# Optimization experiments

Hardware: AMD Instinct MI355X
Metric: run time of the kernel (lower is better)

## Reference

```python
import jax, jax.numpy as jnp
import numpy as np

N = 50000
E = 800000
IN_C, OUT_C, K = 96, 16, 3
L1 = IN_C - (IN_C - OUT_C) // 3            # 70
L2 = IN_C - (2 * (IN_C - OUT_C)) // 3      # 43


def setup_inputs() -> dict:
    key = jax.random.key(0)
    ks = jax.random.split(key, 12)
    x = jax.random.normal(ks[0], (N, IN_C), dtype=jnp.float32)
    edge_index = jax.random.randint(ks[1], (2, E), 0, N, dtype=jnp.int64)

    def glorot(k, shape):
        fan_in, fan_out = shape[-2], shape[-1]
        lim = jnp.sqrt(6.0 / (fan_in + fan_out)).astype(jnp.float32)
        return jax.random.uniform(k, shape, jnp.float32, -lim, lim)

    W1 = glorot(ks[2], (K + 1, IN_C, L1)); b1 = jnp.zeros((L1,), jnp.float32)
    W2 = glorot(ks[3], (K + 1, L1, L2));   b2 = jnp.zeros((L2,), jnp.float32)
    Wmu = glorot(ks[4], (L2, OUT_C));      bmu = jnp.zeros((OUT_C,), jnp.float32)
    Wls = glorot(ks[5], (L2, OUT_C));      bls = jnp.zeros((OUT_C,), jnp.float32)
    return {"x": x, "edge_index": edge_index, "W1": W1, "b1": b1,
            "W2": W2, "b2": b2, "Wmu": Wmu, "bmu": bmu, "Wls": Wls, "bls": bls}


def _norm_no_self_loops(row, col):
    # gcn_norm, add_self_loops=False (TAGConv default)
    deg = jax.ops.segment_sum(jnp.ones((E,), jnp.float32), col, num_segments=N)
    dis = jnp.where(deg > 0, jax.lax.rsqrt(jnp.maximum(deg, 1.0)), 0.0)
    return dis[row] * dis[col]  # [E]


def _tag_conv(x, W, b, row, col, norm):
    # out = sum_k A_hat^k x W_k + b
    out = x @ W[0]
    h = x
    for k in range(1, K + 1):
        h = jax.ops.segment_sum(norm[:, None] * h[row], col, num_segments=N)
        out = out + h @ W[k]
    return out + b


def _gcn_conv(x, W, b, row, col, dis2):
    # gcn_norm with self-loops: dis2 = (deg+1)^{-1/2}
    y = x @ W
    norm = dis2[row] * dis2[col]
    agg = jax.ops.segment_sum(norm[:, None] * y[row], col, num_segments=N)
    return agg + (dis2 * dis2)[:, None] * y + b  # self-loop term + bias


def reference(x, edge_index, W1, b1, W2, b2, Wmu, bmu, Wls, bls):
    row, col = edge_index[0], edge_index[1]
    norm = _norm_no_self_loops(row, col)
    h = jax.nn.relu(_tag_conv(x, W1, b1, row, col, norm))
    h = jax.nn.relu(_tag_conv(h, W2, b2, row, col, norm))
    deg = jax.ops.segment_sum(jnp.ones((E,), jnp.float32), col, num_segments=N)
    dis2 = jax.lax.rsqrt(deg + 1.0)  # self-loops added -> deg+1 > 0
    mu = _gcn_conv(h, Wmu, bmu, row, col, dis2)
    logstd = _gcn_conv(h, Wls, bls, row, col, dis2)
    return mu, logstd
```

## Files before the change

### kernel.cpp

```cpp
#include <hip/hip_runtime.h>
#include <hip/hip_fp16.h>

static constexpr int NN  = 50000;
static constexpr int EE  = 800000;
static constexpr int CIN = 96;
static constexpr int L1C = 70, S1 = 72;
static constexpr int L2C = 43, S2P = 48;

static constexpr int NT1 = 18, KS1 = 3;
static constexpr int NT2 = 12, KS2 = 3;
static constexpr int NTH = 2,  KSH = 2;
static constexpr int NU1 = NT1 * KS1 * 64 * 4;
static constexpr int NU2 = NT2 * KS2 * 64 * 4;
static constexpr int NUH = NTH * KSH * 64 * 4;
static constexpr int TUW = NU1 + NU2 + NUH;
static constexpr int NBF = 288 + 192;

static constexpr int NSLICE = 8;
static constexpr int SLICEN = NN / NSLICE;

typedef short bf16x8 __attribute__((ext_vector_type(8)));
typedef float f32x4  __attribute__((ext_vector_type(4)));

__device__ __forceinline__ float bf_lo(unsigned int u) {
    return __uint_as_float(u << 16);
}
__device__ __forceinline__ float bf_hi(unsigned int u) {
    return __uint_as_float(u & 0xffff0000u);
}
__device__ __forceinline__ unsigned int bf_rne_bits(float f) {
    unsigned int u = __float_as_uint(f);
    return u + 0x7fffu + ((u >> 16) & 1u);
}
__device__ __forceinline__ unsigned int pack_bf(float a, float b) {
    return (bf_rne_bits(a) >> 16) | (bf_rne_bits(b) & 0xffff0000u);
}
__device__ __forceinline__ void unpack_bf8(uint4 q, float* f) {
    f[0] = bf_lo(q.x); f[1] = bf_hi(q.x); f[2] = bf_lo(q.y); f[3] = bf_hi(q.y);
    f[4] = bf_lo(q.z); f[5] = bf_hi(q.z); f[6] = bf_lo(q.w); f[7] = bf_hi(q.w);
}

__device__ __forceinline__ int rec_src(unsigned int p) { return (int)(p & 0xffffu); }
__device__ __forceinline__ float rec_w(unsigned int p) {
    return __half2float(__ushort_as_half((unsigned short)(p >> 16)));
}


__global__ void init_kernel(const float* __restrict__ W1, const float* __restrict__ b1,
                            const float* __restrict__ W2, const float* __restrict__ b2,
                            const float* __restrict__ Wmu, const float* __restrict__ Wls,
                            unsigned int* __restrict__ wB, float* __restrict__ bB,
                            int* __restrict__ deg) {
    int i = blockIdx.x * blockDim.x + threadIdx.x;
    if (i < NN) deg[i] = 0;
    if (i < TUW) {
        float v0 = 0.f, v1 = 0.f;
        if (i < NU1) {
            int frag = i >> 2, j = i & 3;
            int l = frag & 63, ts = frag >> 6;
            int s = ts % 3, t = ts / 3;
            int col = t * 16 + (l & 15);
            int kb  = s * 32 + (l >> 4) * 8 + j * 2;
            int img = col / S1, cin = col - img * S1;
            if (cin < L1C) {
                const float* Wp = W1 + ((size_t)img * CIN + kb) * L1C + cin;
                v0 = Wp[0];
                v1 = Wp[L1C];
            }
        } else if (i < NU1 + NU2) {
            int u = i - NU1;
            int frag = u >> 2, j = u & 3;
            int l = frag & 63, ts = frag >> 6;
            int s = ts % 3, t = ts / 3;
            int col = t * 16 + (l & 15);
            int kb  = s * 32 + (l >> 4) * 8 + j * 2;
            int img = col / S2P, cin = col - img * S2P;
            if (cin < L2C) {
                const float* Wp = W2 + ((size_t)img * L1C + kb) * L2C + cin;
                if (kb < L1C)     v0 = Wp[0];
                if (kb + 1 < L1C) v1 = Wp[L2C];
            }
        } else {
            int u = i - NU1 - NU2;
            int frag = u >> 2, j = u & 3;
            int l = frag & 63, ts = frag >> 6;
            int s = ts & 1, t = ts >> 1;
            int col = t * 16 + (l & 15);
            int kb  = s * 32 + (l >> 4) * 8 + j * 2;
            const float* Wsel = (col < 16) ? (Wmu + col) : (Wls + (col - 16));
            if (kb < L2C)     v0 = Wsel[kb * 16];
            if (kb + 1 < L2C) v1 = Wsel[(kb + 1) * 16];
        }
        wB[i] = pack_bf(v0, v1);
    } else if (i < TUW + NBF) {
        int j = i - TUW;
        float v = 0.f;
        if (j < 288) { if (j < L1C) v = b1[j]; }
        else { int c = j - 288; if (c < L2C) v = b2[c]; }
        bB[j] = v;
    }
}

__global__ void hist_kernel(const int* __restrict__ row, const int* __restrict__ col,
                            int* __restrict__ deg, unsigned int* __restrict__ rr, int E) {
    int e = blockIdx.x * blockDim.x + threadIdx.x;
    if (e < E) {
        int c = col[e];
        int rk = atomicAdd(&deg[c], 1);
        rr[e] = ((unsigned int)rk << 16) | (unsigned int)row[e];
    }
}

static constexpr int SB = 256;

__global__ void reduce_kernel(const int* __restrict__ deg, int* __restrict__ bsum, int n) {
    __shared__ int sd[SB];
    int i = blockIdx.x * SB + threadIdx.x;
    sd[threadIdx.x] = (i < n) ? deg[i] : 0;
    __syncthreads();
    for (int s = SB / 2; s > 0; s >>= 1) {
        if (threadIdx.x < s) sd[threadIdx.x] += sd[threadIdx.x + s];
        __syncthreads();
    }
    if (threadIdx.x == 0) bsum[blockIdx.x] = sd[0];
}

__global__ void block_scan_kernel(const int* __restrict__ deg, const int* __restrict__ bsum,
                                  int* __restrict__ off,
                                  float* __restrict__ dis, float* __restrict__ dis2,
                                  int n, int nb) {
    __shared__ int sd[SB];
    __shared__ int bofs;
    int t = threadIdx.x;
    sd[t] = (t < nb && t < (int)blockIdx.x) ? bsum[t] : 0;
    __syncthreads();
    for (int s = SB / 2; s > 0; s >>= 1) {
        if (t < s) sd[t] += sd[t + s];
        __syncthreads();
    }
    if (t == 0) bofs = sd[0];
    __syncthreads();
    int i = blockIdx.x * SB + t;
    int v = (i < n) ? deg[i] : 0;
    sd[t] = v;
    __syncthreads();
    for (int s = 1; s < SB; s <<= 1) {
        int tv = (t >= s) ? sd[t - s] : 0;
        __syncthreads();
        sd[t] += tv;
        __syncthreads();
    }
    if (i < n) {
        int e = bofs + sd[t] - v;
        off[i] = e;
        dis[i]  = (v > 0) ? rsqrtf((float)v) : 0.0f;
        dis2[i] = rsqrtf((float)v + 1.0f);
        if (i == n - 1) off[n] = e + v;
    }
}

__global__ void fill_kernel(const int* __restrict__ col, const unsigned int* __restrict__ rr,
                            const float* __restrict__ dis, const int* __restrict__ off,
                            unsigned int* __restrict__ eTag, int E) {
    int s = blockIdx.x & (NSLICE - 1);
    int nlo = s * SLICEN, nhi = nlo + SLICEN;
    int stride = (gridDim.x >> 3) * blockDim.x;
    for (int e = (blockIdx.x >> 3) * blockDim.x + threadIdx.x; e < E; e += stride) {
        int c = col[e];
        if (c >= nlo && c < nhi) {
            unsigned int u = rr[e];
            int r = (int)(u & 0xffffu);
            int pos = off[c] + (int)(u >> 16);
            unsigned short h = __half_as_ushort(__float2half(dis[r] * dis[c]));
            eTag[pos] = (unsigned int)r | ((unsigned int)h << 16);
        }
    }
}

template <int C, bool HASADD, bool RELU>
__global__ void aggw_kernel(const unsigned short* __restrict__ in, const unsigned short* addv,
                            unsigned short* out, const int* __restrict__ off,
                            const unsigned int* __restrict__ ep, int n) {
    constexpr int TPN = C / 8;
    int t = blockIdx.x * blockDim.x + threadIdx.x;
    if (t >= n * TPN) return;
    int node = t / TPN;
    int cc = (t - node * TPN) * 8;
    int beg = off[node], end = off[node + 1];
    float a0[8], a1[8];
    #pragma unroll
    for (int j = 0; j < 8; ++j) { a0[j] = 0.f; a1[j] = 0.f; }
    int e = beg;
    for (; e + 4 <= end; e += 4) {
        unsigned int p0 = ep[e], p1 = ep[e + 1], p2 = ep[e + 2], p3 = ep[e + 3];
        float w0 = rec_w(p0), w1 = rec_w(p1), w2 = rec_w(p2), w3 = rec_w(p3);
        uint4 q0 = *reinterpret_cast<const uint4*>(in + (size_t)rec_src(p0) * C + cc);
        uint4 q1 = *reinterpret_cast<const uint4*>(in + (size_t)rec_src(p1) * C + cc);
        uint4 q2 = *reinterpret_cast<const uint4*>(in + (size_t)rec_src(p2) * C + cc);
        uint4 q3 = *reinterpret_cast<const uint4*>(in + (size_t)rec_src(p3) * C + cc);
        float f[8];
        unpack_bf8(q0, f);
        #pragma unroll
        for (int j = 0; j < 8; ++j) a0[j] += w0 * f[j];
        unpack_bf8(q1, f);
        #pragma unroll
        for (int j = 0; j < 8; ++j) a1[j] += w1 * f[j];
        unpack_bf8(q2, f);
        #pragma unroll
        for (int j = 0; j < 8; ++j) a0[j] += w2 * f[j];
        unpack_bf8(q3, f);
        #pragma unroll
        for (int j = 0; j < 8; ++j) a1[j] += w3 * f[j];
    }
    for (; e < end; ++e) {
        unsigned int p = ep[e];
        float w = rec_w(p);
        uint4 q = *reinterpret_cast<const uint4*>(in + (size_t)rec_src(p) * C + cc);
        float f[8];
        unpack_bf8(q, f);
        #pragma unroll
        for (int j = 0; j < 8; ++j) a0[j] += w * f[j];
    }
    float r[8];
    #pragma unroll
    for (int j = 0; j < 8; ++j) r[j] = a0[j] + a1[j];
    if constexpr (HASADD) {
        uint4 qa = *reinterpret_cast<const uint4*>(addv + (size_t)node * C + cc);
        float f[8];
        unpack_bf8(qa, f);
        #pragma unroll
        for (int j = 0; j < 8; ++j) r[j] += f[j];
    }
    if constexpr (RELU) {
        #pragma unroll
        for (int j = 0; j < 8; ++j) r[j] = fmaxf(r[j], 0.f);
    }
    uint4 o;
    o.x = pack_bf(r[0], r[1]); o.y = pack_bf(r[2], r[3]);
    o.z = pack_bf(r[4], r[5]); o.w = pack_bf(r[6], r[7]);
    *reinterpret_cast<uint4*>(out + (size_t)node * C + cc) = o;
}

__global__ void agg_gcn_final_kernel(const unsigned short* __restrict__ yh,
                                     const int* __restrict__ off,
                                     const unsigned int* __restrict__ ep,
                                     const float* __restrict__ dis2,
                                     const float* __restrict__ bmu,
                                     const float* __restrict__ bls,
                                     float* __restrict__ outp, int n) {
    int t = blockIdx.x * blockDim.x + threadIdx.x;
    if (t >= n * 4) return;
    int node = t >> 2;
    int cc = (t & 3) * 8;
    int beg = off[node], end = off[node + 1];
    float a0[8], a1[8];
    #pragma unroll
    for (int j = 0; j < 8; ++j) { a0[j] = 0.f; a1[j] = 0.f; }
    int e = beg;
    for (; e + 2 <= end; e += 2) {
        int s0 = rec_src(ep[e]), s1 = rec_src(ep[e + 1]);
        float w0 = dis2[s0], w1 = dis2[s1];
        uint4 q0 = *reinterpret_cast<const uint4*>(yh + (size_t)s0 * 32 + cc);
        uint4 q1 = *reinterpret_cast<const uint4*>(yh + (size_t)s1 * 32 + cc);
        float f[8];
        unpack_bf8(q0, f);
        #pragma unroll
        for (int j = 0; j < 8; ++j) a0[j] += w0 * f[j];
        unpack_bf8(q1, f);
        #pragma unroll
        for (int j = 0; j < 8; ++j) a1[j] += w1 * f[j];
    }
    for (; e < end; ++e) {
        int s = rec_src(ep[e]);
        float w = dis2[s];
        uint4 q = *reinterpret_cast<const uint4*>(yh + (size_t)s * 32 + cc);
        float f[8];
        unpack_bf8(q, f);
        #pragma unroll
        for (int j = 0; j < 8; ++j) a0[j] += w * f[j];
    }
    float d = dis2[node];
    uint4 qy = *reinterpret_cast<const uint4*>(yh + (size_t)node * 32 + cc);
    float yv[8];
    unpack_bf8(qy, yv);
    const float* bp = (cc < 16) ? (bmu + cc) : (bls + (cc - 16));
    float r[8];
    #pragma unroll
    for (int j = 0; j < 8; ++j)
        r[j] = d * (a0[j] + a1[j]) + d * d * yv[j] + bp[j];
    size_t o = (cc < 16) ? ((size_t)node * 16 + cc)
                         : ((size_t)n * 16 + (size_t)node * 16 + (cc - 16));
    *reinterpret_cast<float4*>(outp + o) = make_float4(r[0], r[1], r[2], r[3]);
    *reinterpret_cast<float4*>(outp + o + 4) = make_float4(r[4], r[5], r[6], r[7]);
}

template <int KS, int NT, int INS, int OIMG, bool CONV, bool BIAS>
__launch_bounds__(256)
__global__ void gemm_kernel(const void* __restrict__ Xv,
                            const unsigned int* __restrict__ Wp,
                            const float* __restrict__ bv,
                            unsigned short* __restrict__ o0,
                            unsigned short* __restrict__ o1,
                            unsigned short* __restrict__ o2,
                            unsigned short* __restrict__ o3,
                            int n) {
    constexpr int WFR = NT * KS * 64;
    constexpr int XFR = KS * 256;
    __shared__ __align__(16) unsigned int Wl[WFR * 4];
    __shared__ __align__(16) unsigned int Xl[(CONV ? 2 : 1) * XFR * 4];

    const int tid = threadIdx.x;
    const int mb = blockIdx.x * 64;

    {
        const uint4* s4 = reinterpret_cast<const uint4*>(Wp);
        uint4* d4 = reinterpret_cast<uint4*>(Wl);
        for (int i = tid; i < WFR; i += 256) d4[i] = s4[i];
    }
    {
        uint4* dx = reinterpret_cast<uint4*>(Xl);
        const int l = tid & 63, w = (tid >> 6) & 3;
        const int m = mb + w * 16 + (l & 15);
        #pragma unroll
        for (int s = 0; s < KS; ++s) {
            int p = s * 256 + tid;
            int k0 = s * 32 + (l >> 4) * 8;
            if constexpr (CONV) {
                bool ok = (m < n);
                const float4* xp = reinterpret_cast<const float4*>(
                    (const float*)Xv + (size_t)m * INS + k0);
                float4 aa = ok ? xp[0] : make_float4(0.f, 0.f, 0.f, 0.f);
                float4 bb = ok ? xp[1] : make_float4(0.f, 0.f, 0.f, 0.f);
                float xv[8] = {aa.x, aa.y, aa.z, aa.w, bb.x, bb.y, bb.z, bb.w};
                unsigned int hb[4], lb[4];
                #pragma unroll
                for (int j = 0; j < 4; ++j) {
                    float a0 = xv[2 * j], a1 = xv[2 * j + 1];
                    unsigned int h0 = bf_rne_bits(a0) & 0xffff0000u;
                    unsigned int h1 = bf_rne_bits(a1) & 0xffff0000u;
                    float r0 = a0 - __uint_as_float(h0);
                    float r1 = a1 - __uint_as_float(h1);
                    hb[j] = (h0 >> 16) | h1;
                    lb[j] = pack_bf(r0, r1);
                }
                dx[p]       = make_uint4(hb[0], hb[1], hb[2], hb[3]);
                dx[XFR + p] = make_uint4(lb[0], lb[1], lb[2], lb[3]);
            } else {
                uint4 v = make_uint4(0u, 0u, 0u, 0u);
                if (m < n && k0 + 8 <= INS)
                    v = *reinterpret_cast<const uint4*>(
                        (const unsigned short*)Xv + (size_t)m * INS + k0);
                dx[p] = v;
            }
        }
    }
    __syncthreads();

    const int w = tid >> 6, lane = tid & 63;
    const int ln = lane & 15, lg = lane >> 4;
    const bf16x8* Wf = reinterpret_cast<const bf16x8*>(Wl);
    const bf16x8* Xf = reinterpret_cast<const bf16x8*>(Xl);

    f32x4 acc[NT];
    #pragma unroll
    for (int t = 0; t < NT; ++t) {
        float b = 0.f;
        if constexpr (BIAS) b = bv[t * 16 + ln];
        acc[t] = (f32x4){b, b, b, b};
    }
    #pragma unroll
    for (int s = 0; s < KS; ++s) {
        bf16x8 ah = Xf[s * 256 + w * 64 + lane];
        bf16x8 al;
        if constexpr (CONV) al = Xf[XFR + s * 256 + w * 64 + lane];
        #pragma unroll
        for (int t = 0; t < NT; ++t) {
            bf16x8 bw = Wf[(t * KS + s) * 64 + lane];
            acc[t] = __builtin_amdgcn_mfma_f32_16x16x32_bf16(ah, bw, acc[t], 0, 0, 0);
            if constexpr (CONV)
                acc[t] = __builtin_amdgcn_mfma_f32_16x16x32_bf16(al, bw, acc[t], 0, 0, 0);
        }
    }
    const int rbase = mb + w * 16 + lg * 4;
    #pragma unroll
    for (int t = 0; t < NT; ++t) {
        int c = t * 16 + ln;
        int img = c / OIMG;
        int colin = c - img * OIMG;
        unsigned short* ob = (img == 0) ? o0 : (img == 1) ? o1 : (img == 2) ? o2 : o3;
        #pragma unroll
        for (int r = 0; r < 4; ++r) {
            int m = rbase + r;
            if (m < n)
                ob[(size_t)m * OIMG + colin] =
                    (unsigned short)(bf_rne_bits(acc[t][r]) >> 16);
        }
    }
}


extern "C" void kernel_launch(void* const* d_in, const int* in_sizes, int n_in,
                              void* d_out, int out_size, void* d_ws, size_t ws_size,
                              hipStream_t stream) {
    const float* x   = (const float*)d_in[0];
    const int*   ei  = (const int*)d_in[1];
    const float* W1  = (const float*)d_in[2];
    const float* b1  = (const float*)d_in[3];
    const float* W2  = (const float*)d_in[4];
    const float* b2  = (const float*)d_in[5];
    const float* Wmu = (const float*)d_in[6];
    const float* bmu = (const float*)d_in[7];
    const float* Wls = (const float*)d_in[8];
    const float* bls = (const float*)d_in[9];
    float* out = (float*)d_out;

    const int N = NN, E = EE;
    const int* row = ei;
    const int* col = ei + E;

    char* p = (char*)d_ws;
    auto alloc = [&](size_t bytes) -> char* {
        char* r = p;
        p += (bytes + 255) & ~(size_t)255;
        return r;
    };
    int*   deg    = (int*)alloc((size_t)N * 4);
    int*   off    = (int*)alloc((size_t)(N + 1) * 4);
    int*   bsum   = (int*)alloc((size_t)256 * 4);
    float* dis    = (float*)alloc((size_t)N * 4);
    float* dis2   = (float*)alloc((size_t)N * 4);
    unsigned int* wB = (unsigned int*)alloc((size_t)TUW * 4);
    float* bB     = (float*)alloc((size_t)NBF * 4);
    unsigned int* eTag = (unsigned int*)alloc((size_t)E * 4);
    unsigned int* rr   = (unsigned int*)alloc((size_t)E * 4);
    unsigned short* y0 = (unsigned short*)alloc((size_t)N * S1 * 2);
    unsigned short* y1 = (unsigned short*)alloc((size_t)N * S1 * 2);
    unsigned short* y2 = (unsigned short*)alloc((size_t)N * S1 * 2);
    unsigned short* y3 = (unsigned short*)alloc((size_t)N * S1 * 2);
    unsigned short* u0 = (unsigned short*)alloc((size_t)N * S2P * 2);
    unsigned short* u1 = (unsigned short*)alloc((size_t)N * S2P * 2);
    unsigned short* u2 = (unsigned short*)alloc((size_t)N * S2P * 2);
    unsigned short* u3 = (unsigned short*)alloc((size_t)N * S2P * 2);
    unsigned short* yh = (unsigned short*)alloc((size_t)N * 32 * 2);

    const unsigned int* W1b = wB;
    const unsigned int* W2b = wB + NU1;
    const unsigned int* Whb = wB + NU1 + NU2;
    const float* bv1 = bB;
    const float* bv2 = bB + 288;

    const int B = 256;
    int gE = (E + B - 1) / B;
    int nb = (N + SB - 1) / SB;

    init_kernel<<<nb, B, 0, stream>>>(W1, b1, W2, b2, Wmu, Wls, wB, bB, deg);
    hist_kernel<<<gE, B, 0, stream>>>(row, col, deg, rr, E);
    reduce_kernel<<<nb, SB, 0, stream>>>(deg, bsum, N);
    block_scan_kernel<<<nb, SB, 0, stream>>>(deg, bsum, off, dis, dis2, N, nb);
    fill_kernel<<<3200, B, 0, stream>>>(col, rr, dis, off, eTag, E);

    int gmm  = (N + 63) / 64;
    int ga72 = (N * (S1 / 8) + B - 1) / B;
    int ga48 = (N * (S2P / 8) + B - 1) / B;
    int gaF  = (N * 4 + B - 1) / B;

    gemm_kernel<3, 9, CIN, S1, true, true ><<<gmm, B, 0, stream>>>(
        x, W1b, bv1, y0, y1, y2, y3, N);
    gemm_kernel<3, 9, CIN, S1, true, false><<<gmm, B, 0, stream>>>(
        x, W1b + NU1 / 2, nullptr, y2, y3, y2, y3, N);
    aggw_kernel<S1, true, false><<<ga72, B, 0, stream>>>(y3, y2, y2, off, eTag, N);
    aggw_kernel<S1, true, false><<<ga72, B, 0, stream>>>(y2, y1, y1, off, eTag, N);
    aggw_kernel<S1, true, true ><<<ga72, B, 0, stream>>>(y1, y0, y0, off, eTag, N);

    gemm_kernel<3, 12, S1, S2P, false, true><<<gmm, B, 0, stream>>>(
        y0, W2b, bv2, u0, u1, u2, u3, N);
    aggw_kernel<S2P, true, false><<<ga48, B, 0, stream>>>(u3, u2, u2, off, eTag, N);
    aggw_kernel<S2P, true, false><<<ga48, B, 0, stream>>>(u2, u1, u1, off, eTag, N);
    aggw_kernel<S2P, true, true ><<<ga48, B, 0, stream>>>(u1, u0, u0, off, eTag, N);

    gemm_kernel<2, 2, S2P, 32, false, false><<<gmm, B, 0, stream>>>(
        u0, Whb, nullptr, yh, yh, yh, yh, N);
    agg_gcn_final_kernel<<<gaF, B, 0, stream>>>(yh, off, eTag, dis2, bmu, bls, out, N);
}
```

Baseline: 320.6 us.

## Sort nodes by degree into bins and aggregate in permuted order

Builds a 64-bin degree histogram during the scan, computes per-block bin offsets with global atomics, and writes a degree-sorted node permutation in a new kernel. All aggregation kernels then index nodes through this permutation so lanes in a wavefront process nodes with similar edge counts, reducing loop divergence. The cost is an extra kernel, extra atomics, and scattered node-row accesses for offsets, residual adds and outputs instead of contiguous ones.

```diff
diff --git a/kernel.cpp b/kernel.cpp
--- a/kernel.cpp
+++ b/kernel.cpp
@@ -50,9 +50,10 @@
                             const float* __restrict__ W2, const float* __restrict__ b2,
                             const float* __restrict__ Wmu, const float* __restrict__ Wls,
                             unsigned int* __restrict__ wB, float* __restrict__ bB,
-                            int* __restrict__ deg) {
+                            int* __restrict__ deg, int* __restrict__ gBin) {
     int i = blockIdx.x * blockDim.x + threadIdx.x;
     if (i < NN) deg[i] = 0;
+    if (i < 64) gBin[i] = 0;
     if (i < TUW) {
         float v0 = 0.f, v1 = 0.f;
         if (i < NU1) {
@@ -128,11 +129,14 @@
 __global__ void block_scan_kernel(const int* __restrict__ deg, const int* __restrict__ bsum,
                                   int* __restrict__ off,
                                   float* __restrict__ dis, float* __restrict__ dis2,
+                                  int* __restrict__ gBin, int* __restrict__ blockBase,
                                   int n, int nb) {
     __shared__ int sd[SB];
+    __shared__ int hb[64];
     __shared__ int bofs;
     int t = threadIdx.x;
     sd[t] = (t < nb && t < (int)blockIdx.x) ? bsum[t] : 0;
+    if (t < 64) hb[t] = 0;
     __syncthreads();
     for (int s = SB / 2; s > 0; s >>= 1) {
         if (t < s) sd[t] += sd[t + s];
@@ -142,6 +146,7 @@
     __syncthreads();
     int i = blockIdx.x * SB + t;
     int v = (i < n) ? deg[i] : 0;
+    if (i < n) atomicAdd(&hb[min(v, 63)], 1);
     sd[t] = v;
     __syncthreads();
     for (int s = 1; s < SB; s <<= 1) {
@@ -156,6 +161,32 @@
         dis[i]  = (v > 0) ? rsqrtf((float)v) : 0.0f;
         dis2[i] = rsqrtf((float)v + 1.0f);
         if (i == n - 1) off[n] = e + v;
+    }
+    if (t < 64) {
+        int c = hb[t];
+        blockBase[blockIdx.x * 64 + t] = (c > 0) ? atomicAdd(&gBin[t], c) : 0;
+    }
+}
+
+__global__ void perm_kernel(const int* __restrict__ deg, const int* __restrict__ gBin,
+                            const int* __restrict__ blockBase, int* __restrict__ perm,
+                            int n) {
+    __shared__ int binStart[64];
+    __shared__ int cur[64];
+    int t = threadIdx.x;
+    if (t < 64) { binStart[t] = gBin[t]; cur[t] = 0; }
+    __syncthreads();
+    if (t == 0) {
+        int s = 0;
+        #pragma unroll
+        for (int b = 0; b < 64; ++b) { int c = binStart[b]; binStart[b] = s; s += c; }
+    }
+    __syncthreads();
+    int i = blockIdx.x * SB + t;
+    if (i < n) {
+        int b = min(deg[i], 63);
+        int r = atomicAdd(&cur[b], 1);
+        perm[binStart[b] + blockBase[blockIdx.x * 64 + b] + r] = i;
     }
 }
 
@@ -180,12 +211,14 @@
 template <int C, bool HASADD, bool RELU>
 __global__ void aggw_kernel(const unsigned short* __restrict__ in, const unsigned short* addv,
                             unsigned short* out, const int* __restrict__ off,
-                            const unsigned int* __restrict__ ep, int n) {
+                            const unsigned int* __restrict__ ep,
+                            const int* __restrict__ perm, int n) {
     constexpr int TPN = C / 8;
     int t = blockIdx.x * blockDim.x + threadIdx.x;
     if (t >= n * TPN) return;
-    int node = t / TPN;
-    int cc = (t - node * TPN) * 8;
+    int g = t / TPN;
+    int node = perm[g];
+    int cc = (t - g * TPN) * 8;
     int beg = off[node], end = off[node + 1];
     float a0[8], a1[8];
     #pragma unroll
@@ -247,10 +280,11 @@
                                      const float* __restrict__ dis2,
                                      const float* __restrict__ bmu,
                                      const float* __restrict__ bls,
+                                     const int* __restrict__ perm,
                                      float* __restrict__ outp, int n) {
     int t = blockIdx.x * blockDim.x + threadIdx.x;
     if (t >= n * 4) return;
-    int node = t >> 2;
+    int node = perm[t >> 2];
     int cc = (t & 3) * 8;
     int beg = off[node], end = off[node + 1];
     float a0[8], a1[8];
@@ -433,6 +467,9 @@
     float* bB     = (float*)alloc((size_t)NBF * 4);
     unsigned int* eTag = (unsigned int*)alloc((size_t)E * 4);
     unsigned int* rr   = (unsigned int*)alloc((size_t)E * 4);
+    int*   gBin   = (int*)alloc((size_t)64 * 4);
+    int*   blockBase = (int*)alloc((size_t)256 * 64 * 4);
+    int*   perm   = (int*)alloc((size_t)N * 4);
     unsigned short* y0 = (unsigned short*)alloc((size_t)N * S1 * 2);
     unsigned short* y1 = (unsigned short*)alloc((size_t)N * S1 * 2);
     unsigned short* y2 = (unsigned short*)alloc((size_t)N * S1 * 2);
@@ -453,10 +490,12 @@
     int gE = (E + B - 1) / B;
     int nb = (N + SB - 1) / SB;
 
-    init_kernel<<<nb, B, 0, stream>>>(W1, b1, W2, b2, Wmu, Wls, wB, bB, deg);
+    init_kernel<<<nb, B, 0, stream>>>(W1, b1, W2, b2, Wmu, Wls, wB, bB, deg, gBin);
     hist_kernel<<<gE, B, 0, stream>>>(row, col, deg, rr, E);
     reduce_kernel<<<nb, SB, 0, stream>>>(deg, bsum, N);
-    block_scan_kernel<<<nb, SB, 0, stream>>>(deg, bsum, off, dis, dis2, N, nb);
+    block_scan_kernel<<<nb, SB, 0, stream>>>(deg, bsum, off, dis, dis2,
+                                             gBin, blockBase, N, nb);
+    perm_kernel<<<nb, SB, 0, stream>>>(deg, gBin, blockBase, perm, N);
     fill_kernel<<<3200, B, 0, stream>>>(col, rr, dis, off, eTag, E);
 
     int gmm  = (N + 63) / 64;
@@ -468,17 +507,17 @@
         x, W1b, bv1, y0, y1, y2, y3, N);
     gemm_kernel<3, 9, CIN, S1, true, false><<<gmm, B, 0, stream>>>(
         x, W1b + NU1 / 2, nullptr, y2, y3, y2, y3, N);
-    aggw_kernel<S1, true, false><<<ga72, B, 0, stream>>>(y3, y2, y2, off, eTag, N);
-    aggw_kernel<S1, true, false><<<ga72, B, 0, stream>>>(y2, y1, y1, off, eTag, N);
-    aggw_kernel<S1, true, true ><<<ga72, B, 0, stream>>>(y1, y0, y0, off, eTag, N);
+    aggw_kernel<S1, true, false><<<ga72, B, 0, stream>>>(y3, y2, y2, off, eTag, perm, N);
+    aggw_kernel<S1, true, false><<<ga72, B, 0, stream>>>(y2, y1, y1, off, eTag, perm, N);
+    aggw_kernel<S1, true, true ><<<ga72, B, 0, stream>>>(y1, y0, y0, off, eTag, perm, N);
 
     gemm_kernel<3, 12, S1, S2P, false, true><<<gmm, B, 0, stream>>>(
         y0, W2b, bv2, u0, u1, u2, u3, N);
-    aggw_kernel<S2P, true, false><<<ga48, B, 0, stream>>>(u3, u2, u2, off, eTag, N);
-    aggw_kernel<S2P, true, false><<<ga48, B, 0, stream>>>(u2, u1, u1, off, eTag, N);
-    aggw_kernel<S2P, true, true ><<<ga48, B, 0, stream>>>(u1, u0, u0, off, eTag, N);
+    aggw_kernel<S2P, true, false><<<ga48, B, 0, stream>>>(u3, u2, u2, off, eTag, perm, N);
+    aggw_kernel<S2P, true, false><<<ga48, B, 0, stream>>>(u2, u1, u1, off, eTag, perm, N);
+    aggw_kernel<S2P, true, true ><<<ga48, B, 0, stream>>>(u1, u0, u0, off, eTag, perm, N);
 
     gemm_kernel<2, 2, S2P, 32, false, false><<<gmm, B, 0, stream>>>(
         u0, Whb, nullptr, yh, yh, yh, yh, N);
-    agg_gcn_final_kernel<<<gaF, B, 0, stream>>>(yh, off, eTag, dis2, bmu, bls, out, N);
-}
+    agg_gcn_final_kernel<<<gaF, B, 0, stream>>>(yh, off, eTag, dis2, bmu, bls, perm, out, N);
+}
```

New measurement: 345.4 us. +7.7%, slower.
